# Optimization experiments

Hardware: AMD Instinct MI355X
Metric: run time of the kernel (lower is better)

The kernel has to match this reference:

```python
import jax, jax.numpy as jnp
import numpy as np

B, Q, C = 32, 900, 92
W_CLASS, W_BBOX, W_GIOU = 1.0, 1.0, 1.0
BIG = 100000000.0


def box_cxcywh_to_xyxy(b):
    cx, cy, w, h = b[..., 0], b[..., 1], b[..., 2], b[..., 3]
    return jnp.stack([cx - 0.5 * w, cy - 0.5 * h, cx + 0.5 * w, cy + 0.5 * h], axis=-1)


def pairwise_generalized_box_iou(b1, b2):
    # b1, b2: [B, Q, 4] in xyxy -> [B, Q, Q]
    area1 = (b1[..., 2] - b1[..., 0]) * (b1[..., 3] - b1[..., 1])  # [B,Q]
    area2 = (b2[..., 2] - b2[..., 0]) * (b2[..., 3] - b2[..., 1])  # [B,Q]
    lt = jnp.maximum(b1[:, :, None, :2], b2[:, None, :, :2])  # [B,Q,Q,2]
    rb = jnp.minimum(b1[:, :, None, 2:], b2[:, None, :, 2:])
    wh = jnp.clip(rb - lt, 0.0)
    inter = wh[..., 0] * wh[..., 1]  # [B,Q,Q]
    union = area1[:, :, None] + area2[:, None, :] - inter
    iou = inter / union
    # smallest enclosing box
    lt_e = jnp.minimum(b1[:, :, None, :2], b2[:, None, :, :2])
    rb_e = jnp.maximum(b1[:, :, None, 2:], b2[:, None, :, 2:])
    wh_e = jnp.clip(rb_e - lt_e, 0.0)
    enc = wh_e[..., 0] * wh_e[..., 1]
    return iou - (enc - union) / enc


def setup_inputs() -> dict:
    key = jax.random.key(0)
    k1, k2, k3, k4, k5 = jax.random.split(key, 5)
    return {
        "pred_logits": jax.random.normal(k1, (B, Q, C), dtype=jnp.float32),
        "pred_boxes": jax.random.uniform(k2, (B, Q, 4), dtype=jnp.float32),
        "boxes": jax.random.uniform(k3, (B, Q, 4), dtype=jnp.float32),
        "area": jax.random.uniform(k4, (B, Q), dtype=jnp.float32),
        "labels": jax.random.randint(k5, (B, Q), 0, C),
    }


def reference(pred_logits, pred_boxes, boxes, area, labels):
    b, q, _ = pred_logits.shape
    out_prob = jax.nn.softmax(pred_logits, axis=-1)  # [B,Q,C]
    # cost_class[b,i,j] = -out_prob[b,i,labels[b,j]]
    idx = jnp.broadcast_to(labels[:, None, :], (b, q, q))
    cost_class = -jnp.take_along_axis(out_prob, idx, axis=2)  # [B,Q,Q]
    # pairwise mean-L1 between cxcywh boxes (tf.reduce_mean over last dim)
    cost_bbox = jnp.mean(jnp.abs(pred_boxes[:, :, None, :] - boxes[:, None, :, :]), axis=-1)
    cost_giou = -pairwise_generalized_box_iou(
        box_cxcywh_to_xyxy(pred_boxes), box_cxcywh_to_xyxy(boxes)
    )
    cost = W_BBOX * cost_bbox + W_CLASS * cost_class + W_GIOU * cost_giou
    return jnp.where((area > 0)[:, None, :], cost, BIG)
```

## Files before the change

### kernel.cpp

```cpp
#include <hip/hip_runtime.h>
#include <math.h>

#define Bn   32
#define Qn   900
#define Cn   92
#define WPB  4
#define RW   5
#define RPB  (WPB * RW)
#define BPB  (Qn / RPB)
#define NBLK (Bn * BPB)
#define BLK  256
#define BIGV 100000000.0f
#define NEGINF -3.402823e38f

typedef float f32x4 __attribute__((ext_vector_type(4)));

__global__ __launch_bounds__(BLK) void hungarian_cost_kernel(
    const float* __restrict__ logits,
    const float* __restrict__ pboxes,
    const float* __restrict__ gboxes,
    const float* __restrict__ area,
    const int*   __restrict__ labels,
    float* __restrict__ out)
{
    __shared__ float s_x0[Qn], s_y0[Qn], s_x1[Qn], s_y1[Qn];
    __shared__ unsigned short s_lab[Qn];
    __shared__ float s_pm[WPB][RW][Cn];

    const int blk   = blockIdx.x;
    const int b     = blk / BPB;
    const int rbase = (blk - b * BPB) * RPB;
    const int tid   = threadIdx.x;
    const int w     = tid >> 6;
    const int lane  = tid & 63;

    {
        const float4* gb4 = (const float4*)(gboxes + (size_t)b * Qn * 4);
        const float*  ga  = area   + (size_t)b * Qn;
        const int*    gl  = labels + (size_t)b * Qn;
        for (int j = tid; j < Qn; j += BLK) {
            float4 cc = gb4[j];
            s_x0[j] = cc.x - 0.5f * cc.z;
            s_y0[j] = cc.y - 0.5f * cc.w;
            s_x1[j] = cc.x + 0.5f * cc.z;
            s_y1[j] = cc.y + 0.5f * cc.w;
            s_lab[j] = (unsigned short)(gl[j] | ((ga[j] > 0.0f) ? 0 : 0x8000));
        }
    }

    float px0[RW], py0[RW], px1[RW], py1[RW], pw[RW], ph[RW], pa[RW];
    const int r0 = rbase + w * RW;
    {
        const float4* pb4 = (const float4*)(pboxes + (size_t)b * Qn * 4);
        #pragma unroll
        for (int m = 0; m < RW; ++m) {
            const int r = r0 + m;
            const float* lrow = logits + ((size_t)b * Qn + r) * Cn;
            float e0 = __expf(lrow[lane]);
            float e1 = (lane < Cn - 64) ? __expf(lrow[lane + 64]) : 0.0f;
            float s = e0 + e1;
            #pragma unroll
            for (int off = 32; off; off >>= 1)
                s += __shfl_xor(s, off);
            float inv = __builtin_amdgcn_rcpf(s);
            s_pm[w][m][lane] = __builtin_fmaf(e0, inv, -1.0f);
            if (lane < Cn - 64) s_pm[w][m][lane + 64] = __builtin_fmaf(e1, inv, -1.0f);
            float4 c = pb4[r];
            px0[m] = c.x - 0.5f * c.z;
            py0[m] = c.y - 0.5f * c.w;
            px1[m] = c.x + 0.5f * c.z;
            py1[m] = c.y + 0.5f * c.w;
            pw[m]  = c.z;  ph[m] = c.w;  pa[m] = c.z * c.w;
        }
    }
    __syncthreads();

    float* ob = out + ((size_t)b * Qn + r0) * Qn;
    #pragma unroll
    for (int t = 0; t < 4; ++t) {
        const int jg = lane + 64 * t;
        if (t < 3 || lane < 33) {
            const int j4 = jg * 4;
            const f32x4 X0 = *(const f32x4*)&s_x0[j4];
            const f32x4 Y0 = *(const f32x4*)&s_y0[j4];
            const f32x4 X1 = *(const f32x4*)&s_x1[j4];
            const f32x4 Y1 = *(const f32x4*)&s_y1[j4];
            const ushort4 LBv = *(const ushort4*)&s_lab[j4];

            #pragma unroll
            for (int m = 0; m < RW; ++m) {
                float res[4];
                #pragma unroll
                for (int k = 0; k < 4; ++k) {
                    const float x0 = X0[k], y0 = Y0[k], x1 = X1[k], y1 = Y1[k];
                    const unsigned short lw = (k==0)?LBv.x:(k==1)?LBv.y:(k==2)?LBv.z:LBv.w;
                    const int   lb = lw & 0x7FFF;
                    const float fl = (lw & 0x8000) ? BIGV : NEGINF;
                    const float pm = s_pm[w][m][lb];

                    float dx0 = px0[m] - x0, dy0 = py0[m] - y0;
                    float dx1 = px1[m] - x1, dy1 = py1[m] - y1;
                    float s1 = fabsf(dx0 + dx1) + fabsf(dy0 + dy1);
                    float s2 = fabsf(dx1 - dx0) + fabsf(dy1 - dy0);
                    float bb = __builtin_fmaf(s1, 0.125f, 0.25f * s2);
                    float iwr = fminf(px1[m], x1) - fmaxf(px0[m], x0);
                    float ihr = fminf(py1[m], y1) - fmaxf(py0[m], y0);
                    float inter = fmaxf(iwr, 0.0f) * fmaxf(ihr, 0.0f);
                    float uni = (pa[m] + (x1 - x0) * (y1 - y0)) - inter;
                    float ew = (pw[m] + (x1 - x0)) - iwr;
                    float eh = (ph[m] + (y1 - y0)) - ihr;
                    float enc = ew * eh;
                    float num = __builtin_fmaf(uni, uni, inter * enc);
                    float g = __builtin_fmaf(num, __builtin_amdgcn_rcpf(uni * enc), pm);
                    res[k] = fmaxf(bb - g, fl);
                }
                f32x4 v = { res[0], res[1], res[2], res[3] };
                __builtin_nontemporal_store(v, (f32x4*)(ob + (size_t)m * Qn + j4));
            }
        }
    }
}

extern "C" void kernel_launch(void* const* d_in, const int* in_sizes, int n_in,
                              void* d_out, int out_size, void* d_ws, size_t ws_size,
                              hipStream_t stream) {
    const float* logits = (const float*)d_in[0];
    const float* pboxes = (const float*)d_in[1];
    const float* gboxes = (const float*)d_in[2];
    const float* areas  = (const float*)d_in[3];
    const int*   labels = (const int*)d_in[4];
    float* out = (float*)d_out;

    hungarian_cost_kernel<<<NBLK, BLK, 0, stream>>>(
        logits, pboxes, gboxes, areas, labels, out);
}
```

Baseline: 40.22 us.

## Interleave per-row class probabilities as float4 and rebalance waves per block

Changes the block shape from 4 waves × 5 rows to 5 waves × 4 rows. With four rows per wave, the softmax probabilities for one class can sit in one f32x4, so a single LDS gather per label serves all rows instead of one scalar gather per row and label. It also staggers the column-tile order per wave and block to spread store traffic, and recomputes box width, height and area from registers to cut register use. The cost is a 320-thread block, different occupancy, and slightly more arithmetic in the inner loop.

Result: slower. 51.63 us (+28.4%).

```diff
diff --git a/kernel.cpp b/kernel.cpp
--- a/kernel.cpp
+++ b/kernel.cpp
@@ -4,12 +4,12 @@
 #define Bn   32
 #define Qn   900
 #define Cn   92
-#define WPB  4
-#define RW   5
+#define WPB  5
+#define RW   4
 #define RPB  (WPB * RW)
 #define BPB  (Qn / RPB)
 #define NBLK (Bn * BPB)
-#define BLK  256
+#define BLK  (WPB * 64)
 #define BIGV 100000000.0f
 #define NEGINF -3.402823e38f
 
@@ -25,14 +25,14 @@
 {
     __shared__ float s_x0[Qn], s_y0[Qn], s_x1[Qn], s_y1[Qn];
     __shared__ unsigned short s_lab[Qn];
-    __shared__ float s_pm[WPB][RW][Cn];
+    __shared__ f32x4 s_pm[WPB][Cn];
 
-    const int blk   = blockIdx.x;
-    const int b     = blk / BPB;
+    const int tid  = threadIdx.x;
+    const int w    = tid >> 6;
+    const int lane = tid & 63;
+    const int blk  = blockIdx.x;
+    const int b    = blk / BPB;
     const int rbase = (blk - b * BPB) * RPB;
-    const int tid   = threadIdx.x;
-    const int w     = tid >> 6;
-    const int lane  = tid & 63;
 
     {
         const float4* gb4 = (const float4*)(gboxes + (size_t)b * Qn * 4);
@@ -48,7 +48,7 @@
         }
     }
 
-    float px0[RW], py0[RW], px1[RW], py1[RW], pw[RW], ph[RW], pa[RW];
+    float px0[RW], py0[RW], px1[RW], py1[RW];
     const int r0 = rbase + w * RW;
     {
         const float4* pb4 = (const float4*)(pboxes + (size_t)b * Qn * 4);
@@ -63,40 +63,50 @@
             for (int off = 32; off; off >>= 1)
                 s += __shfl_xor(s, off);
             float inv = __builtin_amdgcn_rcpf(s);
-            s_pm[w][m][lane] = __builtin_fmaf(e0, inv, -1.0f);
-            if (lane < Cn - 64) s_pm[w][m][lane + 64] = __builtin_fmaf(e1, inv, -1.0f);
+            ((float*)&s_pm[w][lane])[m] = __builtin_fmaf(e0, inv, -1.0f);
+            if (lane < Cn - 64)
+                ((float*)&s_pm[w][lane + 64])[m] = __builtin_fmaf(e1, inv, -1.0f);
             float4 c = pb4[r];
             px0[m] = c.x - 0.5f * c.z;
             py0[m] = c.y - 0.5f * c.w;
             px1[m] = c.x + 0.5f * c.z;
             py1[m] = c.y + 0.5f * c.w;
-            pw[m]  = c.z;  ph[m] = c.w;  pa[m] = c.z * c.w;
         }
     }
     __syncthreads();
 
     float* ob = out + ((size_t)b * Qn + r0) * Qn;
+    const int tph = (w + blk) & 3;
     #pragma unroll
-    for (int t = 0; t < 4; ++t) {
-        const int jg = lane + 64 * t;
-        if (t < 3 || lane < 33) {
+    for (int tt = 0; tt < 4; ++tt) {
+        const int t  = (tt + tph) & 3;
+        const int jg = lane + (t << 6);
+        if (jg < 225) {
             const int j4 = jg * 4;
+            const ushort4 LBv = *(const ushort4*)&s_lab[j4];
             const f32x4 X0 = *(const f32x4*)&s_x0[j4];
             const f32x4 Y0 = *(const f32x4*)&s_y0[j4];
             const f32x4 X1 = *(const f32x4*)&s_x1[j4];
             const f32x4 Y1 = *(const f32x4*)&s_y1[j4];
-            const ushort4 LBv = *(const ushort4*)&s_lab[j4];
+
+            f32x4 pmv[4];
+            #pragma unroll
+            for (int k = 0; k < 4; ++k) {
+                const int lw = (k==0)?LBv.x:(k==1)?LBv.y:(k==2)?LBv.z:LBv.w;
+                pmv[k] = s_pm[w][lw & 0x7FFF];
+            }
 
             #pragma unroll
             for (int m = 0; m < RW; ++m) {
+                const float pwm = px1[m] - px0[m];
+                const float phm = py1[m] - py0[m];
+                const float pam = pwm * phm;
                 float res[4];
                 #pragma unroll
                 for (int k = 0; k < 4; ++k) {
                     const float x0 = X0[k], y0 = Y0[k], x1 = X1[k], y1 = Y1[k];
-                    const unsigned short lw = (k==0)?LBv.x:(k==1)?LBv.y:(k==2)?LBv.z:LBv.w;
-                    const int   lb = lw & 0x7FFF;
+                    const int lw = (k==0)?LBv.x:(k==1)?LBv.y:(k==2)?LBv.z:LBv.w;
                     const float fl = (lw & 0x8000) ? BIGV : NEGINF;
-                    const float pm = s_pm[w][m][lb];
 
                     float dx0 = px0[m] - x0, dy0 = py0[m] - y0;
                     float dx1 = px1[m] - x1, dy1 = py1[m] - y1;
@@ -106,12 +116,14 @@
                     float iwr = fminf(px1[m], x1) - fmaxf(px0[m], x0);
                     float ihr = fminf(py1[m], y1) - fmaxf(py0[m], y0);
                     float inter = fmaxf(iwr, 0.0f) * fmaxf(ihr, 0.0f);
-                    float uni = (pa[m] + (x1 - x0) * (y1 - y0)) - inter;
-                    float ew = (pw[m] + (x1 - x0)) - iwr;
-                    float eh = (ph[m] + (y1 - y0)) - ihr;
+                    float wb = x1 - x0, hb = y1 - y0;
+                    float uni = __builtin_fmaf(wb, hb, pam) - inter;
+                    float ew = (pwm + wb) - iwr;
+                    float eh = (phm + hb) - ihr;
                     float enc = ew * eh;
                     float num = __builtin_fmaf(uni, uni, inter * enc);
-                    float g = __builtin_fmaf(num, __builtin_amdgcn_rcpf(uni * enc), pm);
+                    float g = __builtin_fmaf(num, __builtin_amdgcn_rcpf(uni * enc),
+                                             pmv[k][m]);
                     res[k] = fmaxf(bb - g, fl);
                 }
                 f32x4 v = { res[0], res[1], res[2], res[3] };
```
